# Kernel tuning notes

Measured on AMD Instinct MI355X. Metric: run time of the kernel, lower is better.

Reference implementation:

```python
import jax, jax.numpy as jnp
import numpy as np

SAMPLE_RATE = 32000.0
NUM_APPLICATIONS = 3


def _eq_biquad(x, freq, gain, q, sr):
    """torchaudio.functional.equalizer_biquad: peaking EQ biquad + lfilter.
    x: [B, T] float; freq/gain/q: scalars.
    """
    w0 = 2.0 * jnp.pi * freq / sr
    A = jnp.exp(gain / 40.0 * jnp.log(10.0))  # 10 ** (gain / 40)
    alpha = jnp.sin(w0) / (2.0 * q)
    b0 = 1.0 + alpha * A
    b1 = -2.0 * jnp.cos(w0)
    b2 = 1.0 - alpha * A
    a0 = 1.0 + alpha / A
    a1 = -2.0 * jnp.cos(w0)
    a2 = 1.0 - alpha / A
    # normalize by a0 (as torchaudio biquad -> lfilter does)
    b0, b1, b2 = b0 / a0, b1 / a0, b2 / a0
    a1, a2 = a1 / a0, a2 / a0

    B = x.shape[0]
    z = jnp.zeros((B,), x.dtype)

    def step(carry, xn):
        x1, x2, y1, y2 = carry
        yn = b0 * xn + b1 * x1 + b2 * x2 - a1 * y1 - a2 * y2
        return (xn, x1, yn, y1), yn

    # scan over time axis; carry is per-batch state vectors
    _, y = jax.lax.scan(step, (z, z, z, z), x.T)  # y: [T, B]
    return y.T


def setup_inputs() -> dict:
    key = jax.random.key(0)
    k1, k2, k3, k4 = jax.random.split(key, 4)
    clip = jax.random.normal(k1, (128, 160000), dtype=jnp.float32)
    # draws within the module's f/g/q ranges
    freqs = jax.random.uniform(k2, (NUM_APPLICATIONS,), jnp.float32, 100.0, 6000.0)
    gains = jax.random.uniform(k3, (NUM_APPLICATIONS,), jnp.float32, -8.0, 8.0)
    qs = jax.random.uniform(k4, (NUM_APPLICATIONS,), jnp.float32, 1.0, 9.0)
    return {"clip": clip, "freqs": freqs, "gains": gains, "qs": qs}


def reference(clip, freqs, gains, qs):
    x = clip
    for i in range(NUM_APPLICATIONS):
        x = _eq_biquad(x, freqs[i], gains[i], qs[i], SAMPLE_RATE)
    return x
```

## Files before the change

### kernel.cpp

```cpp
#include <hip/hip_runtime.h>
#include <math.h>

#define SRATE 32000.0
#define NB 128
#define NT 160000
#define CL 100
#define NCROW 1600
#define CPB 64
#define SEG 25
#define NBLK (NB * NCROW / CPB)

#ifndef M_PI
#define M_PI 3.14159265358979323846
#endif

__global__ __launch_bounds__(64) void eq_k1(
    const float* __restrict__ fr, const float* __restrict__ gn,
    const float* __restrict__ qs, float* __restrict__ fc,
    float* __restrict__ Hf, float* __restrict__ Gpf)
{
  __shared__ double dc[24];
  __shared__ double Mb[36], Rb[36], Tb[36];
  const int t = threadIdx.x;
  if (t == 0) {
    for (int f = 0; f < 3; ++f) {
      double w0 = 2.0 * M_PI * (double)fr[f] / SRATE;
      double A  = exp((double)gn[f] / 40.0 * log(10.0));
      double al = sin(w0) / (2.0 * (double)qs[f]);
      double cw = cos(w0);
      double a0 = 1.0 + al / A;
      double b0 = (1.0 + al * A) / a0;
      double b1 = -2.0 * cw / a0;
      double b2 = (1.0 - al * A) / a0;
      double a1 = -2.0 * cw / a0;
      double a2 = (1.0 - al / A) / a0;
      dc[f*8+0]=b0; dc[f*8+1]=b1; dc[f*8+2]=b2; dc[f*8+3]=a1; dc[f*8+4]=a2;
      fc[f*8+0]=(float)b0; fc[f*8+1]=(float)b1; fc[f*8+2]=(float)b2;
      fc[f*8+3]=(float)a1; fc[f*8+4]=(float)a2;
    }
  }
  __syncthreads();
  if (t < 6) {
    double s0=0,s1=0,s2=0,s3=0,s4=0,s5=0;
    if (t==0) s0=1; else if (t==1) s1=1; else if (t==2) s2=1;
    else if (t==3) s3=1; else if (t==4) s4=1; else s5=1;
    double y1 = -dc[3]*s0 - dc[4]*s1;
    double y2 = dc[8]*y1 + dc[9]*s0 + dc[10]*s1 - dc[11]*s2 - dc[12]*s3;
    double y3 = dc[16]*y2 + dc[17]*s2 + dc[18]*s3 - dc[19]*s4 - dc[20]*s5;
    Mb[0*6+t] = y1;  Mb[1*6+t] = s0;
    Mb[2*6+t] = y2;  Mb[3*6+t] = s2;
    Mb[4*6+t] = y3;  Mb[5*6+t] = s4;
  }
  if (t < 36) Rb[t] = ((t % 7) == 0) ? 1.0 : 0.0;
  __syncthreads();
  const int i = t / 6, j = t % 6;
  int e = CL;
  while (e) {
    if (e & 1) {
      double acc = 0.0;
      if (t < 36) { for (int k = 0; k < 6; ++k) acc += Rb[i*6+k]*Mb[k*6+j]; Tb[t]=acc; }
      __syncthreads();
      if (t < 36) Rb[t] = Tb[t];
      __syncthreads();
    }
    e >>= 1;
    if (e) {
      double acc = 0.0;
      if (t < 36) { for (int k = 0; k < 6; ++k) acc += Mb[i*6+k]*Mb[k*6+j]; Tb[t]=acc; }
      __syncthreads();
      if (t < 36) Mb[t] = Tb[t];
      __syncthreads();
    }
  }
  if (t < 36) Hf[t] = (float)Rb[t];
  __syncthreads();
  if (t < 36) Mb[t] = Rb[t];
  __syncthreads();
  if (t < 36) Rb[t] = ((t % 7) == 0) ? 1.0 : 0.0;
  __syncthreads();
  e = SEG;
  while (e) {
    if (e & 1) {
      double acc = 0.0;
      if (t < 36) { for (int k = 0; k < 6; ++k) acc += Rb[i*6+k]*Mb[k*6+j]; Tb[t]=acc; }
      __syncthreads();
      if (t < 36) Rb[t] = Tb[t];
      __syncthreads();
    }
    e >>= 1;
    if (e) {
      double acc = 0.0;
      if (t < 36) { for (int k = 0; k < 6; ++k) acc += Mb[i*6+k]*Mb[k*6+j]; Tb[t]=acc; }
      __syncthreads();
      if (t < 36) Mb[t] = Tb[t];
      __syncthreads();
    }
  }
  if (t < 36) Gpf[t] = (float)Rb[t];
  __syncthreads();
  for (int k = 1; k < 6; ++k) {
    double acc = 0.0;
    if (t < 36) { for (int m = 0; m < 6; ++m) acc += Rb[i*6+m]*Rb[m*6+j]; Tb[t]=acc; }
    __syncthreads();
    if (t < 36) Rb[t] = Tb[t];
    __syncthreads();
    if (t < 36) Gpf[k*36+t] = (float)Rb[t];
    __syncthreads();
  }
}


__global__ __launch_bounds__(64) void eq_k2(
    const float* __restrict__ x, const float* __restrict__ fc,
    float* __restrict__ eo)
{
  __shared__ float lds[64 * 128];
  const int l = threadIdx.x;
  const float* xg = x + (size_t)blockIdx.x * (CPB * CL);
  #pragma unroll
  for (int it = 0; it < 25; ++it) {
    int f = it * 64 + l;
    int seg = f / 25, off = f % 25;
    float4 v = *(const float4*)(xg + seg*CL + off*4);
    *(float4*)(&lds[seg*128 + (((off + seg) & 31) << 2)]) = v;
  }
  __syncthreads();
  const int ch = blockIdx.x * CPB + l;
  float x1, x2;
  if (l == 0) {
    if (ch % NCROW == 0) { x1 = 0.f; x2 = 0.f; }
    else { x1 = xg[-1]; x2 = xg[-2]; }
  } else {
    const int ps = l - 1;
    x1 = lds[ps*128 + (((24 + ps) & 31) << 2) + 3];
    x2 = lds[ps*128 + (((24 + ps) & 31) << 2) + 2];
  }
  const float b01=fc[0],  b11=fc[1],  b21=fc[2],  a11=fc[3],  a21=fc[4];
  const float b02=fc[8],  b12=fc[9],  b22=fc[10], a12=fc[11], a22=fc[12];
  const float b03=fc[16], b13=fc[17], b23=fc[18], a13=fc[19], a23=fc[20];
  float y1p=0,y1pp=0,y2p=0,y2pp=0,y3p=0,y3pp=0;
  #pragma unroll
  for (int jq = 0; jq < 25; ++jq) {
    float4 xv = *(const float4*)(&lds[l*128 + (((jq + l) & 31) << 2)]);
    #pragma unroll
    for (int q = 0; q < 4; ++q) {
      const float xn = (q==0)?xv.x:(q==1)?xv.y:(q==2)?xv.z:xv.w;
      float y1 = b01*xn + b11*x1  + b21*x2   - a11*y1p - a21*y1pp;
      float y2 = b02*y1 + b12*y1p + b22*y1pp - a12*y2p - a22*y2pp;
      float y3 = b03*y2 + b13*y2p + b23*y2pp - a13*y3p - a23*y3pp;
      x2=x1; x1=xn;
      y1pp=y1p; y1p=y1; y2pp=y2p; y2p=y2; y3pp=y3p; y3p=y3;
    }
  }
  float* ep = eo + (size_t)ch * 6;
  ep[0]=y1p; ep[1]=y1pp; ep[2]=y2p; ep[3]=y2pp; ep[4]=y3p; ep[5]=y3pp;
}

__global__ __launch_bounds__(64) void eq_k3(
    float* __restrict__ eo, const float* __restrict__ Hf,
    const float* __restrict__ Gpf)
{
  const int row = blockIdx.x, l = threadIdx.x;
  float H[36];
  #pragma unroll
  for (int i = 0; i < 36; ++i) H[i] = Hf[i];
  float* base = eo + ((size_t)row * NCROW + (size_t)l * SEG) * 6;
  float u[6] = {0,0,0,0,0,0};
  for (int j = 0; j < SEG; ++j) {
    const float* ep = base + j*6;
    float ev[6]; 
    #pragma unroll
    for (int i = 0; i < 6; ++i) ev[i] = ep[i];
    float nu[6];
    #pragma unroll
    for (int i = 0; i < 6; ++i) {
      float acc = ev[i];
      #pragma unroll
      for (int k = 0; k < 6; ++k) acc += H[i*6+k]*u[k];
      nu[i] = acc;
    }
    #pragma unroll
    for (int i = 0; i < 6; ++i) u[i] = nu[i];
  }
  float t6[6];
  #pragma unroll
  for (int i = 0; i < 6; ++i) t6[i] = u[i];
  #pragma unroll
  for (int k = 0; k < 6; ++k) {
    float G[36];
    #pragma unroll
    for (int i = 0; i < 36; ++i) G[i] = Gpf[k*36+i];
    float o[6];
    #pragma unroll
    for (int i = 0; i < 6; ++i) o[i] = __shfl_up(t6[i], 1u << k, 64);
    if (l >= (1 << k)) {
      float nt[6];
      #pragma unroll
      for (int i = 0; i < 6; ++i) {
        float acc = t6[i];
        #pragma unroll
        for (int m = 0; m < 6; ++m) acc += G[i*6+m]*o[m];
        nt[i] = acc;
      }
      #pragma unroll
      for (int i = 0; i < 6; ++i) t6[i] = nt[i];
    }
  }
  float s[6];
  #pragma unroll
  for (int i = 0; i < 6; ++i) s[i] = __shfl_up(t6[i], 1, 64);
  if (l == 0) { 
    #pragma unroll
    for (int i = 0; i < 6; ++i) s[i] = 0.f; 
  }
  for (int j = 0; j < SEG; ++j) {
    float* ep = base + j*6;
    float ev[6];
    #pragma unroll
    for (int i = 0; i < 6; ++i) ev[i] = ep[i];
    #pragma unroll
    for (int i = 0; i < 6; ++i) ep[i] = s[i];
    float ns[6];
    #pragma unroll
    for (int i = 0; i < 6; ++i) {
      float acc = ev[i];
      #pragma unroll
      for (int k = 0; k < 6; ++k) acc += H[i*6+k]*s[k];
      ns[i] = acc;
    }
    #pragma unroll
    for (int i = 0; i < 6; ++i) s[i] = ns[i];
  }
}

__global__ __launch_bounds__(64) void eq_k4(
    const float* __restrict__ x, const float* __restrict__ fc,
    const float* __restrict__ sg, float* __restrict__ y)
{
  __shared__ float lds[64 * 128];
  const int l = threadIdx.x;
  const float* xg = x + (size_t)blockIdx.x * (CPB * CL);
  float* yg = y + (size_t)blockIdx.x * (CPB * CL);
  #pragma unroll
  for (int it = 0; it < 25; ++it) {
    int f = it * 64 + l;
    int seg = f / 25, off = f % 25;
    float4 v = *(const float4*)(xg + seg*CL + off*4);
    *(float4*)(&lds[seg*128 + (((off + seg) & 31) << 2)]) = v;
  }
  __syncthreads();
  const int ch = blockIdx.x * CPB + l;
  float x1, x2;
  if (l == 0) {
    if (ch % NCROW == 0) { x1 = 0.f; x2 = 0.f; }
    else { x1 = xg[-1]; x2 = xg[-2]; }
  } else {
    const int ps = l - 1;
    x1 = lds[ps*128 + (((24 + ps) & 31) << 2) + 3];
    x2 = lds[ps*128 + (((24 + ps) & 31) << 2) + 2];
  }
  __syncthreads();
  const float b01=fc[0],  b11=fc[1],  b21=fc[2],  a11=fc[3],  a21=fc[4];
  const float b02=fc[8],  b12=fc[9],  b22=fc[10], a12=fc[11], a22=fc[12];
  const float b03=fc[16], b13=fc[17], b23=fc[18], a13=fc[19], a23=fc[20];
  const float* sp = sg + (size_t)ch * 6;
  float y1p=sp[0], y1pp=sp[1], y2p=sp[2], y2pp=sp[3], y3p=sp[4], y3pp=sp[5];
  #pragma unroll
  for (int jq = 0; jq < 25; ++jq) {
    float4 xv = *(const float4*)(&lds[l*128 + (((jq + l) & 31) << 2)]);
    float4 yv;
    #pragma unroll
    for (int q = 0; q < 4; ++q) {
      const float xn = (q==0)?xv.x:(q==1)?xv.y:(q==2)?xv.z:xv.w;
      float y1 = b01*xn + b11*x1  + b21*x2   - a11*y1p - a21*y1pp;
      float y2 = b02*y1 + b12*y1p + b22*y1pp - a12*y2p - a22*y2pp;
      float y3 = b03*y2 + b13*y2p + b23*y2pp - a13*y3p - a23*y3pp;
      x2=x1; x1=xn;
      y1pp=y1p; y1p=y1; y2pp=y2p; y2p=y2; y3pp=y3p; y3p=y3;
      if (q==0) yv.x=y3; else if (q==1) yv.y=y3; else if (q==2) yv.z=y3; else yv.w=y3;
    }
    *(float4*)(&lds[l*128 + (((jq + l) & 31) << 2)]) = yv;
  }
  __syncthreads();
  #pragma unroll
  for (int it = 0; it < 25; ++it) {
    int f = it * 64 + l;
    int seg = f / 25, off = f % 25;
    float4 v = *(const float4*)(&lds[seg*128 + (((off + seg) & 31) << 2)]);
    *(float4*)(yg + seg*CL + off*4) = v;
  }
}

extern "C" void kernel_launch(void* const* d_in, const int* in_sizes, int n_in,
                              void* d_out, int out_size, void* d_ws, size_t ws_size,
                              hipStream_t stream) {
  const float* clip = (const float*)d_in[0];
  const float* fr   = (const float*)d_in[1];
  const float* gn   = (const float*)d_in[2];
  const float* qs   = (const float*)d_in[3];
  float* out = (float*)d_out;
  char* ws = (char*)d_ws;
  float* fc  = (float*)ws;
  float* Hf  = (float*)(ws + 256);
  float* Gpf = (float*)(ws + 512);
  float* eo  = (float*)(ws + 4096);

  eq_k1<<<1, 64, 0, stream>>>(fr, gn, qs, fc, Hf, Gpf);
  eq_k2<<<NBLK, 64, 0, stream>>>(clip, fc, eo);
  eq_k3<<<NB, 64, 0, stream>>>(eo, Hf, Gpf);
  eq_k4<<<NBLK, 64, 0, stream>>>(clip, fc, eo, out);
}
```

Before: 88.16 us.

## Fuse three scan kernels into single-pass kernel with decoupled lookback

Replaces the three-pass chunked IIR scan (local end-states, per-row carry propagation, re-run with carries) with one kernel. Each tile gets a dynamic ticket via an atomic counter, computes its local end states, does an in-wave prefix with the H^k powers, and publishes its aggregate with a release flag. It then spin-waits on earlier tiles in the same row and folds their aggregates with H^64. The input stays in LDS between the two filter passes, which avoids rereading the clip and the extra launches. The cost is serial lookback over up to 24 predecessors and spin-wait latency.

```diff
diff --git a/kernel.cpp b/kernel.cpp
--- a/kernel.cpp
+++ b/kernel.cpp
@@ -5,23 +5,31 @@
 #define NB 128
 #define NT 160000
 #define CL 100
-#define NCROW 1600
 #define CPB 64
-#define SEG 25
-#define NBLK (NB * NCROW / CPB)
+#define TPR 25
+#define NTILE 3200
 
 #ifndef M_PI
 #define M_PI 3.14159265358979323846
 #endif
 
-__global__ __launch_bounds__(64) void eq_k1(
+#define WS_FC    0
+#define WS_G     64
+#define WS_H64   280
+#define WS_CNT   320
+#define WS_FLAGS 384
+#define WS_LBUF  4096
+
+__global__ __launch_bounds__(256) void eq_init(
     const float* __restrict__ fr, const float* __restrict__ gn,
-    const float* __restrict__ qs, float* __restrict__ fc,
-    float* __restrict__ Hf, float* __restrict__ Gpf)
+    const float* __restrict__ qs, float* __restrict__ ws)
 {
   __shared__ double dc[24];
   __shared__ double Mb[36], Rb[36], Tb[36];
   const int t = threadIdx.x;
+  int* wsi = (int*)ws;
+  for (int i = t; i < NTILE; i += 256) wsi[WS_FLAGS + i] = 0;
+  if (t == 0) wsi[WS_CNT] = 0;
   if (t == 0) {
     for (int f = 0; f < 3; ++f) {
       double w0 = 2.0 * M_PI * (double)fr[f] / SRATE;
@@ -29,14 +37,11 @@
       double al = sin(w0) / (2.0 * (double)qs[f]);
       double cw = cos(w0);
       double a0 = 1.0 + al / A;
-      double b0 = (1.0 + al * A) / a0;
-      double b1 = -2.0 * cw / a0;
-      double b2 = (1.0 - al * A) / a0;
-      double a1 = -2.0 * cw / a0;
-      double a2 = (1.0 - al / A) / a0;
-      dc[f*8+0]=b0; dc[f*8+1]=b1; dc[f*8+2]=b2; dc[f*8+3]=a1; dc[f*8+4]=a2;
-      fc[f*8+0]=(float)b0; fc[f*8+1]=(float)b1; fc[f*8+2]=(float)b2;
-      fc[f*8+3]=(float)a1; fc[f*8+4]=(float)a2;
+      double b0 = (1.0 + al*A)/a0, b1 = -2.0*cw/a0, b2 = (1.0 - al*A)/a0;
+      double A1 = -2.0*cw/a0,      A2 = (1.0 - al/A)/a0;
+      dc[f*8+0]=b0; dc[f*8+1]=b1; dc[f*8+2]=b2; dc[f*8+3]=A1; dc[f*8+4]=A2;
+      ws[WS_FC+f*5+0]=(float)b0; ws[WS_FC+f*5+1]=(float)b1; ws[WS_FC+f*5+2]=(float)b2;
+      ws[WS_FC+f*5+3]=(float)A1; ws[WS_FC+f*5+4]=(float)A2;
     }
   }
   __syncthreads();
@@ -47,9 +52,7 @@
     double y1 = -dc[3]*s0 - dc[4]*s1;
     double y2 = dc[8]*y1 + dc[9]*s0 + dc[10]*s1 - dc[11]*s2 - dc[12]*s3;
     double y3 = dc[16]*y2 + dc[17]*s2 + dc[18]*s3 - dc[19]*s4 - dc[20]*s5;
-    Mb[0*6+t] = y1;  Mb[1*6+t] = s0;
-    Mb[2*6+t] = y2;  Mb[3*6+t] = s2;
-    Mb[4*6+t] = y3;  Mb[5*6+t] = s4;
+    Mb[0*6+t]=y1; Mb[1*6+t]=s0; Mb[2*6+t]=y2; Mb[3*6+t]=s2; Mb[4*6+t]=y3; Mb[5*6+t]=s4;
   }
   if (t < 36) Rb[t] = ((t % 7) == 0) ? 1.0 : 0.0;
   __syncthreads();
@@ -72,220 +75,203 @@
       __syncthreads();
     }
   }
-  if (t < 36) Hf[t] = (float)Rb[t];
-  __syncthreads();
-  if (t < 36) Mb[t] = Rb[t];
-  __syncthreads();
-  if (t < 36) Rb[t] = ((t % 7) == 0) ? 1.0 : 0.0;
-  __syncthreads();
-  e = SEG;
-  while (e) {
-    if (e & 1) {
-      double acc = 0.0;
-      if (t < 36) { for (int k = 0; k < 6; ++k) acc += Rb[i*6+k]*Mb[k*6+j]; Tb[t]=acc; }
-      __syncthreads();
-      if (t < 36) Rb[t] = Tb[t];
-      __syncthreads();
-    }
-    e >>= 1;
-    if (e) {
-      double acc = 0.0;
-      if (t < 36) { for (int k = 0; k < 6; ++k) acc += Mb[i*6+k]*Mb[k*6+j]; Tb[t]=acc; }
-      __syncthreads();
-      if (t < 36) Mb[t] = Tb[t];
-      __syncthreads();
-    }
-  }
-  if (t < 36) Gpf[t] = (float)Rb[t];
-  __syncthreads();
-  for (int k = 1; k < 6; ++k) {
+  if (t < 36) ws[WS_G + t] = (float)Rb[t];
+  __syncthreads();
+  for (int k = 1; k <= 6; ++k) {
     double acc = 0.0;
     if (t < 36) { for (int m = 0; m < 6; ++m) acc += Rb[i*6+m]*Rb[m*6+j]; Tb[t]=acc; }
     __syncthreads();
     if (t < 36) Rb[t] = Tb[t];
     __syncthreads();
-    if (t < 36) Gpf[k*36+t] = (float)Rb[t];
+    if (t < 36) {
+      if (k <= 5) ws[WS_G + k*36 + t] = (float)Rb[t];
+      else        ws[WS_H64 + t]      = (float)Rb[t];
+    }
     __syncthreads();
   }
 }
 
-
-__global__ __launch_bounds__(64) void eq_k2(
-    const float* __restrict__ x, const float* __restrict__ fc,
-    float* __restrict__ eo)
+__global__ __launch_bounds__(64) void eq_main(
+    const float* __restrict__ x, float* __restrict__ y,
+    const float* __restrict__ cst,
+    int* __restrict__ flags, float* __restrict__ lbuf)
 {
   __shared__ float lds[64 * 128];
+  __shared__ int s_t;
   const int l = threadIdx.x;
-  const float* xg = x + (size_t)blockIdx.x * (CPB * CL);
+  if (l == 0) s_t = atomicAdd((int*)&((int*)cst)[WS_CNT], 1);
+  __syncthreads();
+  const int t = s_t;
+  const int idx = t % TPR;
+  const float* xg = x + (size_t)t * (CPB * CL);
+
   #pragma unroll
   for (int it = 0; it < 25; ++it) {
-    int f = it * 64 + l;
-    int seg = f / 25, off = f % 25;
+    int f = it * 64 + l, seg = f / 25, off = f % 25;
     float4 v = *(const float4*)(xg + seg*CL + off*4);
     *(float4*)(&lds[seg*128 + (((off + seg) & 31) << 2)]) = v;
   }
-  __syncthreads();
-  const int ch = blockIdx.x * CPB + l;
-  float x1, x2;
+  const float c0=cst[WS_FC+0], c1=cst[WS_FC+1], c2=cst[WS_FC+2], c3=cst[WS_FC+3], c4=cst[WS_FC+4];
+  const float c5=cst[WS_FC+5], c6=cst[WS_FC+6], c7=cst[WS_FC+7], c8=cst[WS_FC+8], c9=cst[WS_FC+9];
+  const float cA=cst[WS_FC+10],cB=cst[WS_FC+11],cC=cst[WS_FC+12],cD=cst[WS_FC+13],cE=cst[WS_FC+14];
+  __syncthreads();
+
+  float xh1, xh2;
   if (l == 0) {
-    if (ch % NCROW == 0) { x1 = 0.f; x2 = 0.f; }
-    else { x1 = xg[-1]; x2 = xg[-2]; }
+    if (idx == 0) { xh1 = 0.f; xh2 = 0.f; }
+    else { xh1 = xg[-1]; xh2 = xg[-2]; }
   } else {
     const int ps = l - 1;
-    x1 = lds[ps*128 + (((24 + ps) & 31) << 2) + 3];
-    x2 = lds[ps*128 + (((24 + ps) & 31) << 2) + 2];
-  }
-  const float b01=fc[0],  b11=fc[1],  b21=fc[2],  a11=fc[3],  a21=fc[4];
-  const float b02=fc[8],  b12=fc[9],  b22=fc[10], a12=fc[11], a22=fc[12];
-  const float b03=fc[16], b13=fc[17], b23=fc[18], a13=fc[19], a23=fc[20];
-  float y1p=0,y1pp=0,y2p=0,y2pp=0,y3p=0,y3pp=0;
-  #pragma unroll
-  for (int jq = 0; jq < 25; ++jq) {
-    float4 xv = *(const float4*)(&lds[l*128 + (((jq + l) & 31) << 2)]);
-    #pragma unroll
-    for (int q = 0; q < 4; ++q) {
-      const float xn = (q==0)?xv.x:(q==1)?xv.y:(q==2)?xv.z:xv.w;
-      float y1 = b01*xn + b11*x1  + b21*x2   - a11*y1p - a21*y1pp;
-      float y2 = b02*y1 + b12*y1p + b22*y1pp - a12*y2p - a22*y2pp;
-      float y3 = b03*y2 + b13*y2p + b23*y2pp - a13*y3p - a23*y3pp;
-      x2=x1; x1=xn;
-      y1pp=y1p; y1p=y1; y2pp=y2p; y2p=y2; y3pp=y3p; y3p=y3;
-    }
-  }
-  float* ep = eo + (size_t)ch * 6;
-  ep[0]=y1p; ep[1]=y1pp; ep[2]=y2p; ep[3]=y2pp; ep[4]=y3p; ep[5]=y3pp;
-}
-
-__global__ __launch_bounds__(64) void eq_k3(
-    float* __restrict__ eo, const float* __restrict__ Hf,
-    const float* __restrict__ Gpf)
-{
-  const int row = blockIdx.x, l = threadIdx.x;
-  float H[36];
-  #pragma unroll
-  for (int i = 0; i < 36; ++i) H[i] = Hf[i];
-  float* base = eo + ((size_t)row * NCROW + (size_t)l * SEG) * 6;
-  float u[6] = {0,0,0,0,0,0};
-  for (int j = 0; j < SEG; ++j) {
-    const float* ep = base + j*6;
-    float ev[6]; 
-    #pragma unroll
-    for (int i = 0; i < 6; ++i) ev[i] = ep[i];
-    float nu[6];
+    xh1 = lds[ps*128 + (((24 + ps) & 31) << 2) + 3];
+    xh2 = lds[ps*128 + (((24 + ps) & 31) << 2) + 2];
+  }
+
+  float e6[6];
+  {
+    float x1=xh1, x2=xh2, y1p=0,y1pp=0,y2p=0,y2pp=0,y3p=0,y3pp=0;
+    #pragma unroll
+    for (int jq = 0; jq < 25; ++jq) {
+      float4 xv = *(const float4*)(&lds[l*128 + (((jq + l) & 31) << 2)]);
+      #pragma unroll
+      for (int q = 0; q < 4; ++q) {
+        const float xn = (q==0)?xv.x:(q==1)?xv.y:(q==2)?xv.z:xv.w;
+        float y1 = c0*xn + c1*x1  + c2*x2   - c3*y1p - c4*y1pp;
+        float y2 = c5*y1 + c6*y1p + c7*y1pp - c8*y2p - c9*y2pp;
+        float y3 = cA*y2 + cB*y2p + cC*y2pp - cD*y3p - cE*y3pp;
+        x2=x1; x1=xn;
+        y1pp=y1p; y1p=y1; y2pp=y2p; y2p=y2; y3pp=y3p; y3p=y3;
+      }
+    }
+    e6[0]=y1p; e6[1]=y1pp; e6[2]=y2p; e6[3]=y2pp; e6[4]=y3p; e6[5]=y3pp;
+  }
+
+  float v6[6];
+  #pragma unroll
+  for (int i = 0; i < 6; ++i) v6[i] = e6[i];
+  #pragma unroll
+  for (int k = 0; k < 6; ++k) {
+    const float* G = cst + WS_G + k*36;
+    float o[6];
+    #pragma unroll
+    for (int i = 0; i < 6; ++i) o[i] = __shfl_up(v6[i], 1u << k, 64);
+    if (l >= (1 << k)) {
+      float nv[6];
+      #pragma unroll
+      for (int i = 0; i < 6; ++i) {
+        float a = v6[i];
+        #pragma unroll
+        for (int m = 0; m < 6; ++m) a += G[i*6+m]*o[m];
+        nv[i] = a;
+      }
+      #pragma unroll
+      for (int i = 0; i < 6; ++i) v6[i] = nv[i];
+    }
+  }
+  {
+    float Lv = 0.f;
+    if (l < 6) Lv = __shfl(v6[l], 63, 64);
+  }
+  float Lg[6];
+  #pragma unroll
+  for (int i = 0; i < 6; ++i) Lg[i] = __shfl(v6[i], 63, 64);
+  if (l < 6) lbuf[(size_t)t*6 + l] = Lg[l];
+  __threadfence();
+  if (l == 0) __hip_atomic_store(&flags[t], 1, __ATOMIC_RELEASE, __HIP_MEMORY_SCOPE_AGENT);
+
+  float sg[6] = {0.f,0.f,0.f,0.f,0.f,0.f};
+  if (idx > 0) {
+    const int rowstart = t - idx;
+    if (l < idx) {
+      while (__hip_atomic_load(&flags[rowstart + l], __ATOMIC_RELAXED,
+                               __HIP_MEMORY_SCOPE_AGENT) == 0)
+        __builtin_amdgcn_s_sleep(2);
+    }
+    __threadfence();
+    float Hm[36];
+    #pragma unroll
+    for (int i = 0; i < 36; ++i) Hm[i] = cst[WS_H64 + i];
+    for (int p = rowstart; p < t; ++p) {
+      const float* Lp = lbuf + (size_t)p*6;
+      float ns[6];
+      #pragma unroll
+      for (int i = 0; i < 6; ++i) {
+        float a = Lp[i];
+        #pragma unroll
+        for (int m = 0; m < 6; ++m) a += Hm[i*6+m]*sg[m];
+        ns[i] = a;
+      }
+      #pragma unroll
+      for (int i = 0; i < 6; ++i) sg[i] = ns[i];
+    }
+  }
+
+  if (l == 0) {
+    const float* Hc = cst + WS_G;
+    float ne[6];
     #pragma unroll
     for (int i = 0; i < 6; ++i) {
-      float acc = ev[i];
-      #pragma unroll
-      for (int k = 0; k < 6; ++k) acc += H[i*6+k]*u[k];
-      nu[i] = acc;
-    }
-    #pragma unroll
-    for (int i = 0; i < 6; ++i) u[i] = nu[i];
-  }
-  float t6[6];
-  #pragma unroll
-  for (int i = 0; i < 6; ++i) t6[i] = u[i];
+      float a = e6[i];
+      #pragma unroll
+      for (int m = 0; m < 6; ++m) a += Hc[i*6+m]*sg[m];
+      ne[i] = a;
+    }
+    #pragma unroll
+    for (int i = 0; i < 6; ++i) e6[i] = ne[i];
+  }
+  #pragma unroll
+  for (int i = 0; i < 6; ++i) v6[i] = e6[i];
   #pragma unroll
   for (int k = 0; k < 6; ++k) {
-    float G[36];
-    #pragma unroll
-    for (int i = 0; i < 36; ++i) G[i] = Gpf[k*36+i];
+    const float* G = cst + WS_G + k*36;
     float o[6];
     #pragma unroll
-    for (int i = 0; i < 6; ++i) o[i] = __shfl_up(t6[i], 1u << k, 64);
+    for (int i = 0; i < 6; ++i) o[i] = __shfl_up(v6[i], 1u << k, 64);
     if (l >= (1 << k)) {
-      float nt[6];
+      float nv[6];
       #pragma unroll
       for (int i = 0; i < 6; ++i) {
-        float acc = t6[i];
+        float a = v6[i];
         #pragma unroll
-        for (int m = 0; m < 6; ++m) acc += G[i*6+m]*o[m];
-        nt[i] = acc;
-      }
-      #pragma unroll
-      for (int i = 0; i < 6; ++i) t6[i] = nt[i];
-    }
-  }
-  float s[6];
-  #pragma unroll
-  for (int i = 0; i < 6; ++i) s[i] = __shfl_up(t6[i], 1, 64);
-  if (l == 0) { 
-    #pragma unroll
-    for (int i = 0; i < 6; ++i) s[i] = 0.f; 
-  }
-  for (int j = 0; j < SEG; ++j) {
-    float* ep = base + j*6;
-    float ev[6];
-    #pragma unroll
-    for (int i = 0; i < 6; ++i) ev[i] = ep[i];
-    #pragma unroll
-    for (int i = 0; i < 6; ++i) ep[i] = s[i];
-    float ns[6];
-    #pragma unroll
-    for (int i = 0; i < 6; ++i) {
-      float acc = ev[i];
-      #pragma unroll
-      for (int k = 0; k < 6; ++k) acc += H[i*6+k]*s[k];
-      ns[i] = acc;
-    }
-    #pragma unroll
-    for (int i = 0; i < 6; ++i) s[i] = ns[i];
-  }
-}
-
-__global__ __launch_bounds__(64) void eq_k4(
-    const float* __restrict__ x, const float* __restrict__ fc,
-    const float* __restrict__ sg, float* __restrict__ y)
-{
-  __shared__ float lds[64 * 128];
-  const int l = threadIdx.x;
-  const float* xg = x + (size_t)blockIdx.x * (CPB * CL);
-  float* yg = y + (size_t)blockIdx.x * (CPB * CL);
+        for (int m = 0; m < 6; ++m) a += G[i*6+m]*o[m];
+        nv[i] = a;
+      }
+      #pragma unroll
+      for (int i = 0; i < 6; ++i) v6[i] = nv[i];
+    }
+  }
+  float en[6];
+  #pragma unroll
+  for (int i = 0; i < 6; ++i) en[i] = __shfl_up(v6[i], 1, 64);
+  if (l == 0) {
+    #pragma unroll
+    for (int i = 0; i < 6; ++i) en[i] = sg[i];
+  }
+
+  {
+    float x1=xh1, x2=xh2;
+    float y1p=en[0], y1pp=en[1], y2p=en[2], y2pp=en[3], y3p=en[4], y3pp=en[5];
+    #pragma unroll
+    for (int jq = 0; jq < 25; ++jq) {
+      float4 xv = *(const float4*)(&lds[l*128 + (((jq + l) & 31) << 2)]);
+      float4 yv;
+      #pragma unroll
+      for (int q = 0; q < 4; ++q) {
+        const float xn = (q==0)?xv.x:(q==1)?xv.y:(q==2)?xv.z:xv.w;
+        float y1 = c0*xn + c1*x1  + c2*x2   - c3*y1p - c4*y1pp;
+        float y2 = c5*y1 + c6*y1p + c7*y1pp - c8*y2p - c9*y2pp;
+        float y3 = cA*y2 + cB*y2p + cC*y2pp - cD*y3p - cE*y3pp;
+        x2=x1; x1=xn;
+        y1pp=y1p; y1p=y1; y2pp=y2p; y2p=y2; y3pp=y3p; y3p=y3;
+        if (q==0) yv.x=y3; else if (q==1) yv.y=y3; else if (q==2) yv.z=y3; else yv.w=y3;
+      }
+      *(float4*)(&lds[l*128 + (((jq + l) & 31) << 2)]) = yv;
+    }
+  }
+  __syncthreads();
+  float* yg = y + (size_t)t * (CPB * CL);
   #pragma unroll
   for (int it = 0; it < 25; ++it) {
-    int f = it * 64 + l;
-    int seg = f / 25, off = f % 25;
-    float4 v = *(const float4*)(xg + seg*CL + off*4);
-    *(float4*)(&lds[seg*128 + (((off + seg) & 31) << 2)]) = v;
-  }
-  __syncthreads();
-  const int ch = blockIdx.x * CPB + l;
-  float x1, x2;
-  if (l == 0) {
-    if (ch % NCROW == 0) { x1 = 0.f; x2 = 0.f; }
-    else { x1 = xg[-1]; x2 = xg[-2]; }
-  } else {
-    const int ps = l - 1;
-    x1 = lds[ps*128 + (((24 + ps) & 31) << 2) + 3];
-    x2 = lds[ps*128 + (((24 + ps) & 31) << 2) + 2];
-  }
-  __syncthreads();
-  const float b01=fc[0],  b11=fc[1],  b21=fc[2],  a11=fc[3],  a21=fc[4];
-  const float b02=fc[8],  b12=fc[9],  b22=fc[10], a12=fc[11], a22=fc[12];
-  const float b03=fc[16], b13=fc[17], b23=fc[18], a13=fc[19], a23=fc[20];
-  const float* sp = sg + (size_t)ch * 6;
-  float y1p=sp[0], y1pp=sp[1], y2p=sp[2], y2pp=sp[3], y3p=sp[4], y3pp=sp[5];
-  #pragma unroll
-  for (int jq = 0; jq < 25; ++jq) {
-    float4 xv = *(const float4*)(&lds[l*128 + (((jq + l) & 31) << 2)]);
-    float4 yv;
-    #pragma unroll
-    for (int q = 0; q < 4; ++q) {
-      const float xn = (q==0)?xv.x:(q==1)?xv.y:(q==2)?xv.z:xv.w;
-      float y1 = b01*xn + b11*x1  + b21*x2   - a11*y1p - a21*y1pp;
-      float y2 = b02*y1 + b12*y1p + b22*y1pp - a12*y2p - a22*y2pp;
-      float y3 = b03*y2 + b13*y2p + b23*y2pp - a13*y3p - a23*y3pp;
-      x2=x1; x1=xn;
-      y1pp=y1p; y1p=y1; y2pp=y2p; y2p=y2; y3pp=y3p; y3p=y3;
-      if (q==0) yv.x=y3; else if (q==1) yv.y=y3; else if (q==2) yv.z=y3; else yv.w=y3;
-    }
-    *(float4*)(&lds[l*128 + (((jq + l) & 31) << 2)]) = yv;
-  }
-  __syncthreads();
-  #pragma unroll
-  for (int it = 0; it < 25; ++it) {
-    int f = it * 64 + l;
-    int seg = f / 25, off = f % 25;
+    int f = it * 64 + l, seg = f / 25, off = f % 25;
     float4 v = *(const float4*)(&lds[seg*128 + (((off + seg) & 31) << 2)]);
     *(float4*)(yg + seg*CL + off*4) = v;
   }
@@ -299,14 +285,10 @@
   const float* gn   = (const float*)d_in[2];
   const float* qs   = (const float*)d_in[3];
   float* out = (float*)d_out;
-  char* ws = (char*)d_ws;
-  float* fc  = (float*)ws;
-  float* Hf  = (float*)(ws + 256);
-  float* Gpf = (float*)(ws + 512);
-  float* eo  = (float*)(ws + 4096);
-
-  eq_k1<<<1, 64, 0, stream>>>(fr, gn, qs, fc, Hf, Gpf);
-  eq_k2<<<NBLK, 64, 0, stream>>>(clip, fc, eo);
-  eq_k3<<<NB, 64, 0, stream>>>(eo, Hf, Gpf);
-  eq_k4<<<NBLK, 64, 0, stream>>>(clip, fc, eo, out);
+  float* ws  = (float*)d_ws;
+  int*   wsi = (int*)d_ws;
+
+  eq_init<<<1, 256, 0, stream>>>(fr, gn, qs, ws);
+  eq_main<<<NTILE, 64, 0, stream>>>(clip, out, ws,
+                                    wsi + WS_FLAGS, ws + WS_LBUF);
 }
```

Measured after the change: 272.0 us. 209% more time.

## Fold coefficient and matrix-power setup into scan kernels and transpose carry layout

Applied to the files above, without the earlier changes.

Removes the single-block setup kernel. Each block of the chunk kernels now recomputes the biquad coefficients in float32, and each row block of the carry-propagation kernel recomputes the transition matrix powers itself. The chunk-end states are written padded to 8 floats in a plane-major transposed layout, so the row scan reads them coalesced with float4 loads, and the propagated states are written back in a separate padded buffer. This saves one launch and its serial latency, but every block redoes the setup work, and the coefficients now come from float32 maths instead of double, which may shift accuracy slightly.

```diff
diff --git a/kernel.cpp b/kernel.cpp
--- a/kernel.cpp
+++ b/kernel.cpp
@@ -1,143 +1,67 @@
 #include <hip/hip_runtime.h>
 #include <math.h>
 
-#define SRATE 32000.0
+#define SRATE 32000.f
 #define NB 128
 #define NT 160000
 #define CL 100
+#define CPB 64
+#define TPR 25
+#define NTILE 3200
 #define NCROW 1600
-#define CPB 64
 #define SEG 25
-#define NBLK (NB * NCROW / CPB)
 
 #ifndef M_PI
 #define M_PI 3.14159265358979323846
 #endif
 
-__global__ __launch_bounds__(64) void eq_k1(
-    const float* __restrict__ fr, const float* __restrict__ gn,
-    const float* __restrict__ qs, float* __restrict__ fc,
-    float* __restrict__ Hf, float* __restrict__ Gpf)
+__device__ __forceinline__ void coeffs_f32(
+    const float* fr, const float* gn, const float* qs, float* c)
 {
-  __shared__ double dc[24];
-  __shared__ double Mb[36], Rb[36], Tb[36];
-  const int t = threadIdx.x;
-  if (t == 0) {
-    for (int f = 0; f < 3; ++f) {
-      double w0 = 2.0 * M_PI * (double)fr[f] / SRATE;
-      double A  = exp((double)gn[f] / 40.0 * log(10.0));
-      double al = sin(w0) / (2.0 * (double)qs[f]);
-      double cw = cos(w0);
-      double a0 = 1.0 + al / A;
-      double b0 = (1.0 + al * A) / a0;
-      double b1 = -2.0 * cw / a0;
-      double b2 = (1.0 - al * A) / a0;
-      double a1 = -2.0 * cw / a0;
-      double a2 = (1.0 - al / A) / a0;
-      dc[f*8+0]=b0; dc[f*8+1]=b1; dc[f*8+2]=b2; dc[f*8+3]=a1; dc[f*8+4]=a2;
-      fc[f*8+0]=(float)b0; fc[f*8+1]=(float)b1; fc[f*8+2]=(float)b2;
-      fc[f*8+3]=(float)a1; fc[f*8+4]=(float)a2;
-    }
-  }
-  __syncthreads();
-  if (t < 6) {
-    double s0=0,s1=0,s2=0,s3=0,s4=0,s5=0;
-    if (t==0) s0=1; else if (t==1) s1=1; else if (t==2) s2=1;
-    else if (t==3) s3=1; else if (t==4) s4=1; else s5=1;
-    double y1 = -dc[3]*s0 - dc[4]*s1;
-    double y2 = dc[8]*y1 + dc[9]*s0 + dc[10]*s1 - dc[11]*s2 - dc[12]*s3;
-    double y3 = dc[16]*y2 + dc[17]*s2 + dc[18]*s3 - dc[19]*s4 - dc[20]*s5;
-    Mb[0*6+t] = y1;  Mb[1*6+t] = s0;
-    Mb[2*6+t] = y2;  Mb[3*6+t] = s2;
-    Mb[4*6+t] = y3;  Mb[5*6+t] = s4;
-  }
-  if (t < 36) Rb[t] = ((t % 7) == 0) ? 1.0 : 0.0;
-  __syncthreads();
-  const int i = t / 6, j = t % 6;
-  int e = CL;
-  while (e) {
-    if (e & 1) {
-      double acc = 0.0;
-      if (t < 36) { for (int k = 0; k < 6; ++k) acc += Rb[i*6+k]*Mb[k*6+j]; Tb[t]=acc; }
-      __syncthreads();
-      if (t < 36) Rb[t] = Tb[t];
-      __syncthreads();
-    }
-    e >>= 1;
-    if (e) {
-      double acc = 0.0;
-      if (t < 36) { for (int k = 0; k < 6; ++k) acc += Mb[i*6+k]*Mb[k*6+j]; Tb[t]=acc; }
-      __syncthreads();
-      if (t < 36) Mb[t] = Tb[t];
-      __syncthreads();
-    }
-  }
-  if (t < 36) Hf[t] = (float)Rb[t];
-  __syncthreads();
-  if (t < 36) Mb[t] = Rb[t];
-  __syncthreads();
-  if (t < 36) Rb[t] = ((t % 7) == 0) ? 1.0 : 0.0;
-  __syncthreads();
-  e = SEG;
-  while (e) {
-    if (e & 1) {
-      double acc = 0.0;
-      if (t < 36) { for (int k = 0; k < 6; ++k) acc += Rb[i*6+k]*Mb[k*6+j]; Tb[t]=acc; }
-      __syncthreads();
-      if (t < 36) Rb[t] = Tb[t];
-      __syncthreads();
-    }
-    e >>= 1;
-    if (e) {
-      double acc = 0.0;
-      if (t < 36) { for (int k = 0; k < 6; ++k) acc += Mb[i*6+k]*Mb[k*6+j]; Tb[t]=acc; }
-      __syncthreads();
-      if (t < 36) Mb[t] = Tb[t];
-      __syncthreads();
-    }
-  }
-  if (t < 36) Gpf[t] = (float)Rb[t];
-  __syncthreads();
-  for (int k = 1; k < 6; ++k) {
-    double acc = 0.0;
-    if (t < 36) { for (int m = 0; m < 6; ++m) acc += Rb[i*6+m]*Rb[m*6+j]; Tb[t]=acc; }
-    __syncthreads();
-    if (t < 36) Rb[t] = Tb[t];
-    __syncthreads();
-    if (t < 36) Gpf[k*36+t] = (float)Rb[t];
-    __syncthreads();
-  }
-}
-
-
-__global__ __launch_bounds__(64) void eq_k2(
-    const float* __restrict__ x, const float* __restrict__ fc,
-    float* __restrict__ eo)
+  #pragma unroll
+  for (int f = 0; f < 3; ++f) {
+    float w0 = 2.f * (float)M_PI * fr[f] / SRATE;
+    float A  = expf(gn[f] * (2.302585093f / 40.f));
+    float al = sinf(w0) / (2.f * qs[f]);
+    float cw = cosf(w0);
+    float a0 = 1.f + al / A;
+    c[f*5+0] = (1.f + al*A) / a0;
+    c[f*5+1] = -2.f * cw / a0;
+    c[f*5+2] = (1.f - al*A) / a0;
+    c[f*5+3] = -2.f * cw / a0;
+    c[f*5+4] = (1.f - al/A) / a0;
+  }
+}
+
+
+__global__ __launch_bounds__(64) void eq_a(
+    const float* __restrict__ x, const float* __restrict__ fr,
+    const float* __restrict__ gn, const float* __restrict__ qs,
+    float* __restrict__ eoT)
 {
   __shared__ float lds[64 * 128];
   const int l = threadIdx.x;
-  const float* xg = x + (size_t)blockIdx.x * (CPB * CL);
+  const int t = blockIdx.x;
+  const int row = t / TPR, g = t % TPR;
+  float c[15];
+  coeffs_f32(fr, gn, qs, c);
+  const float* xg = x + (size_t)t * (CPB * CL);
   #pragma unroll
   for (int it = 0; it < 25; ++it) {
-    int f = it * 64 + l;
-    int seg = f / 25, off = f % 25;
+    int f = it * 64 + l, seg = f / 25, off = f % 25;
     float4 v = *(const float4*)(xg + seg*CL + off*4);
     *(float4*)(&lds[seg*128 + (((off + seg) & 31) << 2)]) = v;
   }
   __syncthreads();
-  const int ch = blockIdx.x * CPB + l;
   float x1, x2;
   if (l == 0) {
-    if (ch % NCROW == 0) { x1 = 0.f; x2 = 0.f; }
+    if (g == 0) { x1 = 0.f; x2 = 0.f; }
     else { x1 = xg[-1]; x2 = xg[-2]; }
   } else {
     const int ps = l - 1;
     x1 = lds[ps*128 + (((24 + ps) & 31) << 2) + 3];
     x2 = lds[ps*128 + (((24 + ps) & 31) << 2) + 2];
   }
-  const float b01=fc[0],  b11=fc[1],  b21=fc[2],  a11=fc[3],  a21=fc[4];
-  const float b02=fc[8],  b12=fc[9],  b22=fc[10], a12=fc[11], a22=fc[12];
-  const float b03=fc[16], b13=fc[17], b23=fc[18], a13=fc[19], a23=fc[20];
   float y1p=0,y1pp=0,y2p=0,y2pp=0,y3p=0,y3pp=0;
   #pragma unroll
   for (int jq = 0; jq < 25; ++jq) {
@@ -145,126 +69,200 @@
     #pragma unroll
     for (int q = 0; q < 4; ++q) {
       const float xn = (q==0)?xv.x:(q==1)?xv.y:(q==2)?xv.z:xv.w;
-      float y1 = b01*xn + b11*x1  + b21*x2   - a11*y1p - a21*y1pp;
-      float y2 = b02*y1 + b12*y1p + b22*y1pp - a12*y2p - a22*y2pp;
-      float y3 = b03*y2 + b13*y2p + b23*y2pp - a13*y3p - a23*y3pp;
+      float y1 = c[0]*xn + c[1]*x1  + c[2]*x2   - c[3]*y1p  - c[4]*y1pp;
+      float y2 = c[5]*y1 + c[6]*y1p + c[7]*y1pp - c[8]*y2p  - c[9]*y2pp;
+      float y3 = c[10]*y2 + c[11]*y2p + c[12]*y2pp - c[13]*y3p - c[14]*y3pp;
       x2=x1; x1=xn;
       y1pp=y1p; y1p=y1; y2pp=y2p; y2p=y2; y3pp=y3p; y3p=y3;
     }
   }
-  float* ep = eo + (size_t)ch * 6;
-  ep[0]=y1p; ep[1]=y1pp; ep[2]=y2p; ep[3]=y2pp; ep[4]=y3p; ep[5]=y3pp;
-}
-
-__global__ __launch_bounds__(64) void eq_k3(
-    float* __restrict__ eo, const float* __restrict__ Hf,
-    const float* __restrict__ Gpf)
+  const int ci = g * 64 + l;
+  const int plane = ci % 25, slot = ci / 25;
+  float* ep = eoT + ((size_t)(row*25 + plane)*64 + slot)*8;
+  float4 r0; r0.x=y1p; r0.y=y1pp; r0.z=y2p; r0.w=y2pp;
+  float4 r1; r1.x=y3p; r1.y=y3pp; r1.z=0.f; r1.w=0.f;
+  *(float4*)ep = r0; *(float4*)(ep+4) = r1;
+}
+
+__global__ __launch_bounds__(64) void eq_b(
+    const float* __restrict__ fr, const float* __restrict__ gn,
+    const float* __restrict__ qs, const float* __restrict__ eoT,
+    float* __restrict__ sgD)
 {
-  const int row = blockIdx.x, l = threadIdx.x;
+  __shared__ double Mb[36], Rb[36], Tb[36];
+  __shared__ float Hs[36], Gs[6*36];
+  const int l = threadIdx.x, row = blockIdx.x;
+  float c[15];
+  coeffs_f32(fr, gn, qs, c);
+  if (l < 6) {
+    double s0=0,s1=0,s2=0,s3=0,s4=0,s5=0;
+    if (l==0) s0=1; else if (l==1) s1=1; else if (l==2) s2=1;
+    else if (l==3) s3=1; else if (l==4) s4=1; else s5=1;
+    double y1 = -(double)c[3]*s0 - (double)c[4]*s1;
+    double y2 = (double)c[5]*y1 + (double)c[6]*s0 + (double)c[7]*s1
+              - (double)c[8]*s2 - (double)c[9]*s3;
+    double y3 = (double)c[10]*y2 + (double)c[11]*s2 + (double)c[12]*s3
+              - (double)c[13]*s4 - (double)c[14]*s5;
+    Mb[0*6+l]=y1; Mb[1*6+l]=s0; Mb[2*6+l]=y2; Mb[3*6+l]=s2; Mb[4*6+l]=y3; Mb[5*6+l]=s4;
+  }
+  if (l < 36) Rb[l] = ((l % 7) == 0) ? 1.0 : 0.0;
+  __syncthreads();
+  const int i = l / 6, j = l % 6;
+  int e = CL;
+  while (e) {
+    if (e & 1) {
+      double acc = 0.0;
+      if (l < 36) { for (int k = 0; k < 6; ++k) acc += Rb[i*6+k]*Mb[k*6+j]; Tb[l]=acc; }
+      __syncthreads();
+      if (l < 36) Rb[l] = Tb[l];
+      __syncthreads();
+    }
+    e >>= 1;
+    if (e) {
+      double acc = 0.0;
+      if (l < 36) { for (int k = 0; k < 6; ++k) acc += Mb[i*6+k]*Mb[k*6+j]; Tb[l]=acc; }
+      __syncthreads();
+      if (l < 36) Mb[l] = Tb[l];
+      __syncthreads();
+    }
+  }
+  if (l < 36) { Hs[l] = (float)Rb[l]; Mb[l] = Rb[l]; }
+  __syncthreads();
+  if (l < 36) Rb[l] = ((l % 7) == 0) ? 1.0 : 0.0;
+  __syncthreads();
+  e = SEG;
+  while (e) {
+    if (e & 1) {
+      double acc = 0.0;
+      if (l < 36) { for (int k = 0; k < 6; ++k) acc += Rb[i*6+k]*Mb[k*6+j]; Tb[l]=acc; }
+      __syncthreads();
+      if (l < 36) Rb[l] = Tb[l];
+      __syncthreads();
+    }
+    e >>= 1;
+    if (e) {
+      double acc = 0.0;
+      if (l < 36) { for (int k = 0; k < 6; ++k) acc += Mb[i*6+k]*Mb[k*6+j]; Tb[l]=acc; }
+      __syncthreads();
+      if (l < 36) Mb[l] = Tb[l];
+      __syncthreads();
+    }
+  }
+  if (l < 36) Gs[l] = (float)Rb[l];
+  __syncthreads();
+  for (int k = 1; k < 6; ++k) {
+    double acc = 0.0;
+    if (l < 36) { for (int m = 0; m < 6; ++m) acc += Rb[i*6+m]*Rb[m*6+j]; Tb[l]=acc; }
+    __syncthreads();
+    if (l < 36) Rb[l] = Tb[l];
+    __syncthreads();
+    if (l < 36) Gs[k*36+l] = (float)Rb[l];
+    __syncthreads();
+  }
+
   float H[36];
   #pragma unroll
-  for (int i = 0; i < 36; ++i) H[i] = Hf[i];
-  float* base = eo + ((size_t)row * NCROW + (size_t)l * SEG) * 6;
+  for (int q = 0; q < 36; ++q) H[q] = Hs[q];
+  const float* rbase = eoT + (size_t)row * (25*64*8);
   float u[6] = {0,0,0,0,0,0};
-  for (int j = 0; j < SEG; ++j) {
-    const float* ep = base + j*6;
-    float ev[6]; 
-    #pragma unroll
-    for (int i = 0; i < 6; ++i) ev[i] = ep[i];
+  for (int jj = 0; jj < SEG; ++jj) {
+    const float* ep = rbase + (size_t)(jj*64 + l)*8;
+    float4 r0 = *(const float4*)ep, r1 = *(const float4*)(ep+4);
+    float ev[6] = {r0.x,r0.y,r0.z,r0.w,r1.x,r1.y};
     float nu[6];
     #pragma unroll
-    for (int i = 0; i < 6; ++i) {
-      float acc = ev[i];
+    for (int q = 0; q < 6; ++q) {
+      float a = ev[q];
       #pragma unroll
-      for (int k = 0; k < 6; ++k) acc += H[i*6+k]*u[k];
-      nu[i] = acc;
-    }
-    #pragma unroll
-    for (int i = 0; i < 6; ++i) u[i] = nu[i];
-  }
-  float t6[6];
-  #pragma unroll
-  for (int i = 0; i < 6; ++i) t6[i] = u[i];
+      for (int m = 0; m < 6; ++m) a += H[q*6+m]*u[m];
+      nu[q] = a;
+    }
+    #pragma unroll
+    for (int q = 0; q < 6; ++q) u[q] = nu[q];
+  }
+  float v6[6];
+  #pragma unroll
+  for (int q = 0; q < 6; ++q) v6[q] = u[q];
   #pragma unroll
   for (int k = 0; k < 6; ++k) {
-    float G[36];
-    #pragma unroll
-    for (int i = 0; i < 36; ++i) G[i] = Gpf[k*36+i];
+    const float* G = Gs + k*36;
     float o[6];
     #pragma unroll
-    for (int i = 0; i < 6; ++i) o[i] = __shfl_up(t6[i], 1u << k, 64);
+    for (int q = 0; q < 6; ++q) o[q] = __shfl_up(v6[q], 1u << k, 64);
     if (l >= (1 << k)) {
-      float nt[6];
+      float nv[6];
       #pragma unroll
-      for (int i = 0; i < 6; ++i) {
-        float acc = t6[i];
+      for (int q = 0; q < 6; ++q) {
+        float a = v6[q];
         #pragma unroll
-        for (int m = 0; m < 6; ++m) acc += G[i*6+m]*o[m];
-        nt[i] = acc;
+        for (int m = 0; m < 6; ++m) a += G[q*6+m]*o[m];
+        nv[q] = a;
       }
       #pragma unroll
-      for (int i = 0; i < 6; ++i) t6[i] = nt[i];
+      for (int q = 0; q < 6; ++q) v6[q] = nv[q];
     }
   }
   float s[6];
   #pragma unroll
-  for (int i = 0; i < 6; ++i) s[i] = __shfl_up(t6[i], 1, 64);
-  if (l == 0) { 
-    #pragma unroll
-    for (int i = 0; i < 6; ++i) s[i] = 0.f; 
-  }
-  for (int j = 0; j < SEG; ++j) {
-    float* ep = base + j*6;
-    float ev[6];
-    #pragma unroll
-    for (int i = 0; i < 6; ++i) ev[i] = ep[i];
-    #pragma unroll
-    for (int i = 0; i < 6; ++i) ep[i] = s[i];
+  for (int q = 0; q < 6; ++q) s[q] = __shfl_up(v6[q], 1, 64);
+  if (l == 0) {
+    #pragma unroll
+    for (int q = 0; q < 6; ++q) s[q] = 0.f;
+  }
+  float* wbase = sgD + (size_t)row * (NCROW*8);
+  for (int jj = 0; jj < SEG; ++jj) {
+    const float* ep = rbase + (size_t)(jj*64 + l)*8;
+    float4 r0 = *(const float4*)(ep), r1 = *(const float4*)(ep+4);
+    float ev[6] = {r0.x,r0.y,r0.z,r0.w,r1.x,r1.y};
+    float* wp = wbase + (size_t)(l*SEG + jj)*8;
+    float4 w0; w0.x=s[0]; w0.y=s[1]; w0.z=s[2]; w0.w=s[3];
+    float4 w1; w1.x=s[4]; w1.y=s[5]; w1.z=0.f; w1.w=0.f;
+    *(float4*)wp = w0; *(float4*)(wp+4) = w1;
     float ns[6];
     #pragma unroll
-    for (int i = 0; i < 6; ++i) {
-      float acc = ev[i];
+    for (int q = 0; q < 6; ++q) {
+      float a = ev[q];
       #pragma unroll
-      for (int k = 0; k < 6; ++k) acc += H[i*6+k]*s[k];
-      ns[i] = acc;
-    }
-    #pragma unroll
-    for (int i = 0; i < 6; ++i) s[i] = ns[i];
-  }
-}
-
-__global__ __launch_bounds__(64) void eq_k4(
-    const float* __restrict__ x, const float* __restrict__ fc,
-    const float* __restrict__ sg, float* __restrict__ y)
+      for (int m = 0; m < 6; ++m) a += H[q*6+m]*s[m];
+      ns[q] = a;
+    }
+    #pragma unroll
+    for (int q = 0; q < 6; ++q) s[q] = ns[q];
+  }
+}
+
+__global__ __launch_bounds__(64) void eq_c(
+    const float* __restrict__ x, const float* __restrict__ fr,
+    const float* __restrict__ gn, const float* __restrict__ qs,
+    const float* __restrict__ sgD, float* __restrict__ y)
 {
   __shared__ float lds[64 * 128];
   const int l = threadIdx.x;
-  const float* xg = x + (size_t)blockIdx.x * (CPB * CL);
-  float* yg = y + (size_t)blockIdx.x * (CPB * CL);
+  const int t = blockIdx.x;
+  const int row = t / TPR, g = t % TPR;
+  float c[15];
+  coeffs_f32(fr, gn, qs, c);
+  const float* xg = x + (size_t)t * (CPB * CL);
+  float* yg = y + (size_t)t * (CPB * CL);
   #pragma unroll
   for (int it = 0; it < 25; ++it) {
-    int f = it * 64 + l;
-    int seg = f / 25, off = f % 25;
+    int f = it * 64 + l, seg = f / 25, off = f % 25;
     float4 v = *(const float4*)(xg + seg*CL + off*4);
     *(float4*)(&lds[seg*128 + (((off + seg) & 31) << 2)]) = v;
   }
   __syncthreads();
-  const int ch = blockIdx.x * CPB + l;
   float x1, x2;
   if (l == 0) {
-    if (ch % NCROW == 0) { x1 = 0.f; x2 = 0.f; }
+    if (g == 0) { x1 = 0.f; x2 = 0.f; }
     else { x1 = xg[-1]; x2 = xg[-2]; }
   } else {
     const int ps = l - 1;
     x1 = lds[ps*128 + (((24 + ps) & 31) << 2) + 3];
     x2 = lds[ps*128 + (((24 + ps) & 31) << 2) + 2];
   }
-  __syncthreads();
-  const float b01=fc[0],  b11=fc[1],  b21=fc[2],  a11=fc[3],  a21=fc[4];
-  const float b02=fc[8],  b12=fc[9],  b22=fc[10], a12=fc[11], a22=fc[12];
-  const float b03=fc[16], b13=fc[17], b23=fc[18], a13=fc[19], a23=fc[20];
-  const float* sp = sg + (size_t)ch * 6;
-  float y1p=sp[0], y1pp=sp[1], y2p=sp[2], y2pp=sp[3], y3p=sp[4], y3pp=sp[5];
+  const float* sp = sgD + ((size_t)row * NCROW + (size_t)(g*64 + l)) * 8;
+  float4 s0 = *(const float4*)sp, s1 = *(const float4*)(sp+4);
+  float y1p=s0.x, y1pp=s0.y, y2p=s0.z, y2pp=s0.w, y3p=s1.x, y3pp=s1.y;
   #pragma unroll
   for (int jq = 0; jq < 25; ++jq) {
     float4 xv = *(const float4*)(&lds[l*128 + (((jq + l) & 31) << 2)]);
@@ -272,9 +270,9 @@
     #pragma unroll
     for (int q = 0; q < 4; ++q) {
       const float xn = (q==0)?xv.x:(q==1)?xv.y:(q==2)?xv.z:xv.w;
-      float y1 = b01*xn + b11*x1  + b21*x2   - a11*y1p - a21*y1pp;
-      float y2 = b02*y1 + b12*y1p + b22*y1pp - a12*y2p - a22*y2pp;
-      float y3 = b03*y2 + b13*y2p + b23*y2pp - a13*y3p - a23*y3pp;
+      float y1 = c[0]*xn + c[1]*x1  + c[2]*x2   - c[3]*y1p  - c[4]*y1pp;
+      float y2 = c[5]*y1 + c[6]*y1p + c[7]*y1pp - c[8]*y2p  - c[9]*y2pp;
+      float y3 = c[10]*y2 + c[11]*y2p + c[12]*y2pp - c[13]*y3p - c[14]*y3pp;
       x2=x1; x1=xn;
       y1pp=y1p; y1p=y1; y2pp=y2p; y2p=y2; y3pp=y3p; y3p=y3;
       if (q==0) yv.x=y3; else if (q==1) yv.y=y3; else if (q==2) yv.z=y3; else yv.w=y3;
@@ -284,8 +282,7 @@
   __syncthreads();
   #pragma unroll
   for (int it = 0; it < 25; ++it) {
-    int f = it * 64 + l;
-    int seg = f / 25, off = f % 25;
+    int f = it * 64 + l, seg = f / 25, off = f % 25;
     float4 v = *(const float4*)(&lds[seg*128 + (((off + seg) & 31) << 2)]);
     *(float4*)(yg + seg*CL + off*4) = v;
   }
@@ -299,14 +296,10 @@
   const float* gn   = (const float*)d_in[2];
   const float* qs   = (const float*)d_in[3];
   float* out = (float*)d_out;
-  char* ws = (char*)d_ws;
-  float* fc  = (float*)ws;
-  float* Hf  = (float*)(ws + 256);
-  float* Gpf = (float*)(ws + 512);
-  float* eo  = (float*)(ws + 4096);
-
-  eq_k1<<<1, 64, 0, stream>>>(fr, gn, qs, fc, Hf, Gpf);
-  eq_k2<<<NBLK, 64, 0, stream>>>(clip, fc, eo);
-  eq_k3<<<NB, 64, 0, stream>>>(eo, Hf, Gpf);
-  eq_k4<<<NBLK, 64, 0, stream>>>(clip, fc, eo, out);
-}
+  float* eoT = (float*)d_ws;
+  float* sgD = eoT + (size_t)NB * NCROW * 8;
+
+  eq_a<<<NTILE, 64, 0, stream>>>(clip, fr, gn, qs, eoT);
+  eq_b<<<NB, 64, 0, stream>>>(fr, gn, qs, eoT, sgD);
+  eq_c<<<NTILE, 64, 0, stream>>>(clip, fr, gn, qs, sgD, out);
+}
```

After: 94.47 us. 7.2% more time.
